# Optimization experiments

Hardware: AMD Instinct MI355X
Metric: run time of the kernel (lower is better)

## Reference

```python
import jax, jax.numpy as jnp
import numpy as np

EPS = 1e-12  # torch F.normalize default eps


def setup_inputs() -> dict:
    key = jax.random.key(0)
    ks = jax.random.split(key, 4)
    b, c, h, w = 2, 192, 256, 256
    num_heads = 4
    x = jax.random.normal(ks[0], (b, c, h, w), dtype=jnp.float32)
    w_qkv = jax.random.normal(ks[1], (3 * c, c), dtype=jnp.float32) * 0.02
    w_dw = jax.random.normal(ks[2], (3 * c, 1, 3, 3), dtype=jnp.float32) * 0.1
    w_proj = jax.random.normal(ks[3], (c, c), dtype=jnp.float32) * 0.02
    temperature = jnp.ones((num_heads, 1, 1), dtype=jnp.float32)
    return {"x": x, "w_qkv": w_qkv, "w_dw": w_dw, "w_proj": w_proj,
            "temperature": temperature, "num_heads": num_heads}


def reference(x, w_qkv, w_dw, w_proj, temperature, num_heads):
    b, c, h, w = x.shape
    ch = c // num_heads
    # 1x1 conv (pointwise GEMM) then depthwise 3x3 conv
    qkv = jnp.einsum('bchw,oc->bohw', x, w_qkv)
    qkv = jax.lax.conv_general_dilated(
        qkv, w_dw, window_strides=(1, 1), padding='SAME',
        dimension_numbers=('NCHW', 'OIHW', 'NCHW'),
        feature_group_count=3 * c)
    q, k, v = jnp.split(qkv, 3, axis=1)
    # b (head c) h w -> b head (c h) w
    def to_heads(t):
        return t.reshape(b, num_heads, ch * h, w)
    q, k, v = to_heads(q), to_heads(k), to_heads(v)
    # L2-normalize over the (c h) axis
    def l2n(t):
        n = jnp.sqrt(jnp.sum(t * t, axis=-2, keepdims=True))
        return t / jnp.maximum(n, EPS)
    q, k = l2n(q), l2n(k)
    # channel-transposed attention over width: attn is (b, head, w, w)
    attn = jnp.einsum('bhcw,bhcv->bhwv', q, k) * temperature[None]
    attn = jax.nn.softmax(attn, axis=-2)  # softmax over dim=-2 as in source
    out = jnp.einsum('bhcw,bhwv->bhcv', v, attn)
    out = out.reshape(b, c, h, w)
    return jnp.einsum('bchw,oc->bohw', out, w_proj)
```

## Files before the change

kernel.cpp:

```cpp
#include <hip/hip_runtime.h>
#include <math.h>

#define HW 65536

typedef float f32x4 __attribute__((ext_vector_type(4)));
typedef short bf16x8 __attribute__((ext_vector_type(8)));
typedef short bf16x4 __attribute__((ext_vector_type(4)));

static constexpr size_t OFF_A0    = 0;
static constexpr size_t OFF_SP    = 50331648;
static constexpr size_t OFF_VOUTT = 100663296;
static constexpr size_t OFF_XQK   = 150994944;
static constexpr size_t OFF_VPL   = 251658240;
static constexpr size_t OFF_PT    = 301989888;
static constexpr size_t OFF_NORMS = 303038464;
static constexpr size_t OFF_WQ    = 303054848;
static constexpr size_t OFF_WP    = 303276032;

__device__ inline float b2f(unsigned short u) { union { unsigned u; float f; } v; v.u = ((unsigned)u) << 16; return v.f; }
__device__ inline unsigned short f2b(float f) {
    union { float f; unsigned u; } v; v.f = f;
    return (unsigned short)((v.u + 0x7fffu + ((v.u >> 16) & 1u)) >> 16);
}

__global__ __launch_bounds__(256) void conv_w(const float* __restrict__ wq, const float* __restrict__ wp,
                                              unsigned short* __restrict__ wqb, unsigned short* __restrict__ wpb)
{
    int t = blockIdx.x * 256 + threadIdx.x;
    int stride = gridDim.x * 256;
    for (int i = t; i < 576 * 192; i += stride) wqb[i] = f2b(wq[i]);
    for (int i = t; i < 192 * 192; i += stride) wpb[i] = f2b(wp[i]);
}

__global__ __launch_bounds__(256) void conv_x(const float* __restrict__ x, unsigned short* __restrict__ xb)
{
    __shared__ unsigned short T[64 * 200];
    int tid = threadIdx.x;
    int b = blockIdx.y;
    long p0 = (long)blockIdx.x * 64;
#pragma unroll
    for (int it = 0; it < 12; ++it) {
        int c = it * 16 + (tid >> 4);
        int px = (tid & 15) * 4;
        float4 v = *(const float4*)(x + ((long)b * 192 + c) * HW + p0 + px);
        T[(px + 0) * 200 + c] = f2b(v.x);
        T[(px + 1) * 200 + c] = f2b(v.y);
        T[(px + 2) * 200 + c] = f2b(v.z);
        T[(px + 3) * 200 + c] = f2b(v.w);
    }
    __syncthreads();
    int px = tid >> 2, q = tid & 3;
    unsigned short* ob = xb + ((long)b * HW + p0 + px) * 192 + q * 48;
#pragma unroll
    for (int e = 0; e < 6; ++e)
        *(bf16x8*)(ob + e * 8) = *(const bf16x8*)&T[px * 200 + q * 48 + e * 8];
}

__global__ __launch_bounds__(256) void gemm_pm2(const unsigned short* __restrict__ Aw,
                                                const unsigned short* __restrict__ Bp,
                                                unsigned short* __restrict__ outb,
                                                float* __restrict__ outf, int Mtiles)
{
    __shared__ unsigned short Bs[128 * 200];
    int tid = threadIdx.x;
    int w = tid >> 6, lane = tid & 63, lg = lane >> 4, li = lane & 15;
    int wm = w >> 1, wn = w & 1;
    long pflat = (long)blockIdx.x * 128;

#pragma unroll
    for (int it = 0; it < 12; ++it) {
        int f = it * 256 + tid;
        int row = f / 24, cs = (f % 24) * 8;
        *(bf16x8*)&Bs[row * 200 + cs] = *(const bf16x8*)(Bp + (pflat + row) * 192 + cs);
    }
    __syncthreads();

    bf16x8 Bf[4][6];
#pragma unroll
    for (int fb = 0; fb < 4; ++fb)
#pragma unroll
        for (int ks = 0; ks < 6; ++ks)
            Bf[fb][ks] = *(const bf16x8*)&Bs[(wn * 64 + fb * 16 + li) * 200 + ks * 32 + lg * 8];

    const int b = (int)(blockIdx.x >> 9);
    const int pxl = ((int)blockIdx.x & 511) * 128 + wn * 64;
    const int Mtot = Mtiles * 64;

    for (int mt = 0; mt < Mtiles; ++mt) {
        int oc0 = mt * 64;
        const unsigned short* ab = Aw + (long)(oc0 + wm * 32 + li) * 192 + lg * 8;
        f32x4 acc[2][4];
#pragma unroll
        for (int i = 0; i < 2; ++i)
#pragma unroll
            for (int j = 0; j < 4; ++j) acc[i][j] = (f32x4){0.f, 0.f, 0.f, 0.f};
#pragma unroll
        for (int ks = 0; ks < 6; ++ks) {
            bf16x8 a0 = *(const bf16x8*)(ab + ks * 32);
            bf16x8 a1 = *(const bf16x8*)(ab + 16 * 192 + ks * 32);
#pragma unroll
            for (int fb = 0; fb < 4; ++fb) {
                acc[0][fb] = __builtin_amdgcn_mfma_f32_16x16x32_bf16(a0, Bf[fb][ks], acc[0][fb], 0, 0, 0);
                acc[1][fb] = __builtin_amdgcn_mfma_f32_16x16x32_bf16(a1, Bf[fb][ks], acc[1][fb], 0, 0, 0);
            }
        }
#pragma unroll
        for (int fa = 0; fa < 2; ++fa) {
            int m = oc0 + wm * 32 + fa * 16 + lg * 4;
#pragma unroll
            for (int fb = 0; fb < 4; ++fb) {
                int px = pxl + fb * 16 + li;
                long base = ((long)b * Mtot + m) * HW + px;
#pragma unroll
                for (int ii = 0; ii < 4; ++ii) {
                    if (outf) outf[base + (long)ii * HW] = acc[fa][fb][ii];
                    else      outb[base + (long)ii * HW] = f2b(acc[fa][fb][ii]);
                }
            }
        }
    }
}

__global__ __launch_bounds__(256) void dwconv2(const unsigned short* __restrict__ in,
                                               const float* __restrict__ wdw,
                                               unsigned short* __restrict__ qkT,
                                               unsigned short* __restrict__ vpl)
{
    __shared__ unsigned short Ls[34 * 272];
    int tid = threadIdx.x;
    int zp = blockIdx.y;
    int b = zp / 576, ch3 = zp % 576;
    int y0 = blockIdx.x * 32;
    const unsigned short* ip = in + (long)zp * HW;
    float w9[9];
#pragma unroll
    for (int t = 0; t < 9; ++t) w9[t] = wdw[ch3 * 9 + t];

    const bf16x8 z8 = (bf16x8){0, 0, 0, 0, 0, 0, 0, 0};
    if (tid < 34)               *(bf16x8*)&Ls[tid * 272] = z8;
    else if (tid < 68)          *(bf16x8*)&Ls[(tid - 34) * 272 + 264] = z8;
#pragma unroll
    for (int it = 0; it < 5; ++it) {
        int task = it * 256 + tid;
        if (task < 1088) {
            int r = task >> 5, seg = task & 31;
            int gy = y0 - 1 + r;
            bf16x8 v = z8;
            if (gy >= 0 && gy < 256) v = *(const bf16x8*)(ip + gy * 256 + seg * 8);
            *(bf16x8*)&Ls[r * 272 + 8 + seg * 8] = v;
        }
    }
    __syncthreads();

    int xg = tid & 63, yg = tid >> 6;
    int x0 = xg * 4;
    float acc[8][4];
#pragma unroll
    for (int yy = 0; yy < 8; ++yy)
#pragma unroll
        for (int xi = 0; xi < 4; ++xi) acc[yy][xi] = 0.f;

#pragma unroll
    for (int rr = 0; rr < 10; ++rr) {
        const unsigned short* lp = &Ls[(yg * 8 + rr) * 272 + 8 + x0];
        bf16x4 A  = *(const bf16x4*)(lp - 4);
        bf16x4 Bv = *(const bf16x4*)(lp);
        bf16x4 Cv = *(const bf16x4*)(lp + 4);
        float f[6] = { b2f((unsigned short)A[3]),  b2f((unsigned short)Bv[0]),
                       b2f((unsigned short)Bv[1]), b2f((unsigned short)Bv[2]),
                       b2f((unsigned short)Bv[3]), b2f((unsigned short)Cv[0]) };
#pragma unroll
        for (int dy = 0; dy < 3; ++dy) {
            int yy = rr - dy;
            if (yy >= 0 && yy < 8) {
#pragma unroll
                for (int dx = 0; dx < 3; ++dx)
#pragma unroll
                    for (int xi = 0; xi < 4; ++xi)
                        acc[yy][xi] = fmaf(w9[dy * 3 + dx], f[dx + xi], acc[yy][xi]);
            }
        }
    }

    if (ch3 < 384) {
        int isk = ch3 >= 192 ? 1 : 0;
        int chq = ch3 - isk * 192;
        int hh = chq / 48, cc = chq % 48;
        long zbase = (long)(b * 8 + isk * 4 + hh) * 3145728L + (long)cc * 256 + y0 + yg * 8;
#pragma unroll
        for (int xi = 0; xi < 4; ++xi) {
            bf16x8 pv;
#pragma unroll
            for (int yy = 0; yy < 8; ++yy) pv[yy] = (short)f2b(acc[yy][xi]);
            *(bf16x8*)(qkT + zbase + (long)(x0 + xi) * 12288) = pv;
        }
    } else {
        unsigned short* ob = vpl + (long)(b * 192 + ch3 - 384) * HW + (long)(y0 + yg * 8) * 256 + x0;
#pragma unroll
        for (int yy = 0; yy < 8; ++yy) {
            bf16x4 pv;
#pragma unroll
            for (int xi = 0; xi < 4; ++xi) pv[xi] = (short)f2b(acc[yy][xi]);
            *(bf16x4*)(ob + yy * 256) = pv;
        }
    }
}

__global__ __launch_bounds__(256) void transpose_bf16(const unsigned short* __restrict__ src,
                                                      unsigned short* __restrict__ dst, int mode)
{
    __shared__ unsigned short T[64][72];
    int tid = threadIdx.x;
    int z = blockIdx.z;
    long so, dofs; int R, C;
    if (mode == 0) {
        int b = z >> 3, isk = (z >> 2) & 1, h = z & 3;
        so = ((long)(b * 576 + isk * 192 + h * 48)) * HW;
        dofs = (long)z * 12288 * 256;
        R = 12288; C = 256;
    } else {
        so = (long)z * 192 * HW;
        dofs = (long)z * HW * 192;
        R = 192; C = HW;
    }
    int r0 = blockIdx.y * 64, c0 = blockIdx.x * 64;
#pragma unroll
    for (int rr = 0; rr < 2; ++rr) {
        int r = rr * 32 + (tid >> 3);
        int cs = (tid & 7) * 8;
        *(bf16x8*)&T[r][cs] = *(const bf16x8*)(src + so + (long)(r0 + r) * C + c0 + cs);
    }
    __syncthreads();
#pragma unroll
    for (int cc = 0; cc < 2; ++cc) {
        int c = cc * 32 + (tid >> 3);
        int rs = (tid & 7) * 8;
        bf16x8 v;
#pragma unroll
        for (int e = 0; e < 8; ++e) v[e] = (short)T[rs + e][c];
        *(bf16x8*)(dst + dofs + (long)(c0 + c) * R + r0 + rs) = v;
    }
}

__global__ __launch_bounds__(256) void norms_k(const unsigned short* __restrict__ qkT, float* __restrict__ norms)
{
    int i = blockIdx.x, z = blockIdx.y;
    const unsigned short* p = qkT + ((long)z * 256 + i) * 12288 + threadIdx.x * 8;
    float s = 0.f;
#pragma unroll
    for (int it = 0; it < 6; ++it) {
        bf16x8 v = *(const bf16x8*)(p + it * 2048);
#pragma unroll
        for (int e = 0; e < 8; ++e) { float f = b2f((unsigned short)v[e]); s = fmaf(f, f, s); }
    }
    for (int off = 32; off > 0; off >>= 1) s += __shfl_down(s, off, 64);
    __shared__ float r4[4];
    if ((threadIdx.x & 63) == 0) r4[threadIdx.x >> 6] = s;
    __syncthreads();
    if (threadIdx.x == 0) {
        float t = r4[0] + r4[1] + r4[2] + r4[3];
        norms[z * 256 + i] = 1.0f / fmaxf(sqrtf(t), 1e-12f);
    }
}

__global__ __launch_bounds__(256) void attn_qk(const unsigned short* __restrict__ qkT, float* __restrict__ Sp)
{
    __shared__ unsigned short Qs[128 * 40];
    __shared__ unsigned short Ks[128 * 40];
    int tid = threadIdx.x;
    int z = blockIdx.z; int bh = z >> 4, sk = z & 15; int b = bh >> 2, h = bh & 3;
    const unsigned short* qT = qkT + (long)(b * 8 + h) * 3145728;
    const unsigned short* kT = qkT + (long)(b * 8 + 4 + h) * 3145728;
    int i0 = blockIdx.x * 128, j0 = blockIdx.y * 128;
    int w = tid >> 6, lane = tid & 63, lg = lane >> 4, li = lane & 15;
    int wm = w >> 1, wn = w & 1;
    int srow = tid >> 2, sseg = (tid & 3) * 8;
    long qoff = (long)(i0 + srow) * 12288 + sk * 768 + sseg;
    long koff = (long)(j0 + srow) * 12288 + sk * 768 + sseg;

    f32x4 acc[4][4];
#pragma unroll
    for (int i = 0; i < 4; ++i)
#pragma unroll
        for (int j = 0; j < 4; ++j) acc[i][j] = (f32x4){0.f, 0.f, 0.f, 0.f};

    bf16x8 qr0 = *(const bf16x8*)(qT + qoff);
    bf16x8 qr1 = *(const bf16x8*)(qT + qoff + (long)64 * 12288);
    bf16x8 kr0 = *(const bf16x8*)(kT + koff);
    bf16x8 kr1 = *(const bf16x8*)(kT + koff + (long)64 * 12288);

#pragma unroll 1
    for (int ks = 0; ks < 24; ++ks) {
        *(bf16x8*)&Qs[srow * 40 + sseg] = qr0;
        *(bf16x8*)&Qs[(64 + srow) * 40 + sseg] = qr1;
        *(bf16x8*)&Ks[srow * 40 + sseg] = kr0;
        *(bf16x8*)&Ks[(64 + srow) * 40 + sseg] = kr1;
        if (ks < 23) {
            long o = (long)(ks + 1) * 32;
            qr0 = *(const bf16x8*)(qT + qoff + o);
            qr1 = *(const bf16x8*)(qT + qoff + (long)64 * 12288 + o);
            kr0 = *(const bf16x8*)(kT + koff + o);
            kr1 = *(const bf16x8*)(kT + koff + (long)64 * 12288 + o);
        }
        __syncthreads();
        bf16x8 af[4], bfr[4];
#pragma unroll
        for (int fa = 0; fa < 4; ++fa)
            af[fa] = *(const bf16x8*)&Qs[(wm * 64 + fa * 16 + li) * 40 + lg * 8];
#pragma unroll
        for (int fb = 0; fb < 4; ++fb)
            bfr[fb] = *(const bf16x8*)&Ks[(wn * 64 + fb * 16 + li) * 40 + lg * 8];
#pragma unroll
        for (int fa = 0; fa < 4; ++fa)
#pragma unroll
            for (int fb = 0; fb < 4; ++fb)
                acc[fa][fb] = __builtin_amdgcn_mfma_f32_16x16x32_bf16(af[fa], bfr[fb], acc[fa][fb], 0, 0, 0);
        __syncthreads();
    }

    float* op = Sp + ((long)(sk * 8 + bh) << 16);
#pragma unroll
    for (int fa = 0; fa < 4; ++fa) {
        int i = i0 + wm * 64 + fa * 16 + lg * 4;
#pragma unroll
        for (int fb = 0; fb < 4; ++fb) {
            int j = j0 + wn * 64 + fb * 16 + li;
#pragma unroll
            for (int ii = 0; ii < 4; ++ii)
                op[(long)(i + ii) * 256 + j] = acc[fa][fb][ii];
        }
    }
}

__global__ __launch_bounds__(256) void softmax_k(const float* __restrict__ Sp, const float* __restrict__ norms,
                                                 const float* __restrict__ temp, unsigned short* __restrict__ Pt)
{
    __shared__ float Sd[256 * 9];
    __shared__ float red[32 * 9];
    int tid = threadIdx.x;
    int g = blockIdx.x; int bh = g >> 5, jq = g & 31; int b = bh >> 2, h = bh & 3;
    int jl = tid & 7, iq = tid >> 3;
    int j = jq * 8 + jl;
    const float* nq = norms + (b * 8 + h) * 256;
    float invkj = norms[(b * 8 + 4 + h) * 256 + j] * temp[h];
    const float* sp = Sp + (long)bh * HW + j;

    float m = -1e30f;
#pragma unroll
    for (int ii = 0; ii < 8; ++ii) {
        int i = iq * 8 + ii;
        float s = 0.f;
#pragma unroll
        for (int sk = 0; sk < 16; ++sk) s += sp[((long)(sk * 8) << 16) + i * 256];
        float v = s * nq[i] * invkj;
        Sd[i * 9 + jl] = v;
        m = fmaxf(m, v);
    }
    red[iq * 9 + jl] = m;
    __syncthreads();
    m = -1e30f;
#pragma unroll
    for (int s2 = 0; s2 < 32; ++s2) m = fmaxf(m, red[s2 * 9 + jl]);
    __syncthreads();
    float sum = 0.f;
#pragma unroll
    for (int ii = 0; ii < 8; ++ii) sum += __expf(Sd[(iq * 8 + ii) * 9 + jl] - m);
    red[iq * 9 + jl] = sum;
    __syncthreads();
    sum = 0.f;
#pragma unroll
    for (int s2 = 0; s2 < 32; ++s2) sum += red[s2 * 9 + jl];
    float rs = 1.0f / sum;

    int fb = jq >> 1, li2 = (jq & 1) * 8 + jl;
    int ks = iq >> 2, lg = iq & 3;
    unsigned short* pt = Pt + (long)bh * HW + (long)((fb * 8 + ks) * 64 + lg * 16 + li2) * 8;
    bf16x8 pv;
#pragma unroll
    for (int ii = 0; ii < 8; ++ii)
        pv[ii] = (short)f2b(__expf(Sd[(iq * 8 + ii) * 9 + jl] - m) * rs);
    *(bf16x8*)pt = pv;
}

__global__ __launch_bounds__(256) void vattn(const unsigned short* __restrict__ vpl,
                                             const unsigned short* __restrict__ Pt,
                                             unsigned short* __restrict__ vout)
{
    int tid = threadIdx.x;
    int w = tid >> 6, lane = tid & 63, lg = lane >> 4, li = lane & 15;
    int wm = w >> 1, wn = w & 1;
    int m0 = blockIdx.x * 64 + wm * 32;
    int bh = blockIdx.y; int b = bh >> 2, h = bh & 3;
    const unsigned short* V = vpl + (long)(b * 192 + h * 48) * HW;
    const unsigned short* P = Pt + (long)bh * HW + wn * 32768 + lane * 8;

    f32x4 acc[2][8];
#pragma unroll
    for (int i = 0; i < 2; ++i)
#pragma unroll
        for (int j = 0; j < 8; ++j) acc[i][j] = (f32x4){0.f, 0.f, 0.f, 0.f};

#pragma unroll 2
    for (int ks = 0; ks < 8; ++ks) {
        bf16x8 a0 = *(const bf16x8*)(V + (long)(m0 + li) * 256 + ks * 32 + lg * 8);
        bf16x8 a1 = *(const bf16x8*)(V + (long)(m0 + 16 + li) * 256 + ks * 32 + lg * 8);
#pragma unroll
        for (int fb2 = 0; fb2 < 8; ++fb2) {
            bf16x8 bb = *(const bf16x8*)(P + (fb2 * 8 + ks) * 512);
            acc[0][fb2] = __builtin_amdgcn_mfma_f32_16x16x32_bf16(a0, bb, acc[0][fb2], 0, 0, 0);
            acc[1][fb2] = __builtin_amdgcn_mfma_f32_16x16x32_bf16(a1, bb, acc[1][fb2], 0, 0, 0);
        }
    }
    unsigned short* ob = vout + (long)(b * 192 + h * 48) * HW;
#pragma unroll
    for (int fa = 0; fa < 2; ++fa) {
#pragma unroll
        for (int fb2 = 0; fb2 < 8; ++fb2) {
            int j = (wn * 8 + fb2) * 16 + li;
#pragma unroll
            for (int ii = 0; ii < 4; ++ii) {
                int m = m0 + fa * 16 + lg * 4 + ii;
                ob[((long)(m >> 8) << 16) + ((m & 255) << 8) + j] = f2b(acc[fa][fb2][ii]);
            }
        }
    }
}

extern "C" void kernel_launch(void* const* d_in, const int* in_sizes, int n_in,
                              void* d_out, int out_size, void* d_ws, size_t ws_size,
                              hipStream_t stream)
{
    (void)in_sizes; (void)n_in; (void)out_size; (void)ws_size;
    const float* x      = (const float*)d_in[0];
    const float* w_qkv  = (const float*)d_in[1];
    const float* w_dw   = (const float*)d_in[2];
    const float* w_proj = (const float*)d_in[3];
    const float* temp   = (const float*)d_in[4];
    float* out = (float*)d_out;
    char* ws = (char*)d_ws;

    unsigned short* qkv_pre = (unsigned short*)(ws + OFF_A0);
    unsigned short* vout    = (unsigned short*)(ws + OFF_A0);
    float*          Sp      = (float*)(ws + OFF_SP);
    unsigned short* voutT   = (unsigned short*)(ws + OFF_VOUTT);
    unsigned short* xb      = (unsigned short*)(ws + OFF_XQK);
    unsigned short* qkT     = (unsigned short*)(ws + OFF_XQK);
    unsigned short* vpl     = (unsigned short*)(ws + OFF_VPL);
    unsigned short* Pt      = (unsigned short*)(ws + OFF_PT);
    float*          norms   = (float*)(ws + OFF_NORMS);
    unsigned short* wqb     = (unsigned short*)(ws + OFF_WQ);
    unsigned short* wpb     = (unsigned short*)(ws + OFF_WP);

    conv_w<<<64, 256, 0, stream>>>(w_qkv, w_proj, wqb, wpb);
    conv_x<<<dim3(1024, 2), 256, 0, stream>>>(x, xb);
    gemm_pm2<<<1024, 256, 0, stream>>>(wqb, xb, qkv_pre, nullptr, 9);
    dwconv2<<<dim3(8, 1152), 256, 0, stream>>>(qkv_pre, w_dw, qkT, vpl);
    norms_k<<<dim3(256, 16), 256, 0, stream>>>(qkT, norms);
    attn_qk<<<dim3(2, 2, 128), 256, 0, stream>>>(qkT, Sp);
    softmax_k<<<256, 256, 0, stream>>>(Sp, norms, temp, Pt);
    vattn<<<dim3(192, 8), 256, 0, stream>>>(vpl, Pt, vout);
    transpose_bf16<<<dim3(1024, 3, 2), 256, 0, stream>>>(vout, voutT, 1);
    gemm_pm2<<<1024, 256, 0, stream>>>(wpb, voutT, nullptr, out, 3);
}
```

Before: 349.8 us.

## Fuse q/k norm reduction into dwconv epilogue and widen attn_qk tiles

The depthwise conv kernel now computes per-column squared sums of the q/k outputs from its fp32 accumulators, reduces them in shared memory and atomically adds them into a zeroed buffer. A tiny finalize kernel then turns these into inverse norms, replacing the separate norms kernel that re-read all of qkT. attn_qk is also reshaped to 512-thread blocks covering all 256 key columns, so each Q tile is loaded once instead of twice. The cost is extra barriers and atomics in dwconv, plus a larger shared-memory footprint and fewer blocks in attn_qk. Norms now come from unrounded fp32 values, a slight numerical change.

```diff
diff --git a/kernel.cpp b/kernel.cpp
--- a/kernel.cpp
+++ b/kernel.cpp
@@ -7,15 +7,16 @@
 typedef short bf16x8 __attribute__((ext_vector_type(8)));
 typedef short bf16x4 __attribute__((ext_vector_type(4)));
 
-static constexpr size_t OFF_A0    = 0;
-static constexpr size_t OFF_SP    = 50331648;
-static constexpr size_t OFF_VOUTT = 100663296;
-static constexpr size_t OFF_XQK   = 150994944;
-static constexpr size_t OFF_VPL   = 251658240;
-static constexpr size_t OFF_PT    = 301989888;
-static constexpr size_t OFF_NORMS = 303038464;
-static constexpr size_t OFF_WQ    = 303054848;
-static constexpr size_t OFF_WP    = 303276032;
+static constexpr size_t OFF_A0     = 0;
+static constexpr size_t OFF_SP     = 50331648;
+static constexpr size_t OFF_VOUTT  = 100663296;
+static constexpr size_t OFF_XQK    = 150994944;
+static constexpr size_t OFF_VPL    = 251658240;
+static constexpr size_t OFF_PT     = 301989888;
+static constexpr size_t OFF_NORMP  = 303038464;
+static constexpr size_t OFF_WQ     = 303054848;
+static constexpr size_t OFF_WP     = 303276032;
+static constexpr size_t OFF_NORMS  = 303349760;
 
 __device__ inline float b2f(unsigned short u) { union { unsigned u; float f; } v; v.u = ((unsigned)u) << 16; return v.f; }
 __device__ inline unsigned short f2b(float f) {
@@ -124,7 +125,8 @@
 __global__ __launch_bounds__(256) void dwconv2(const unsigned short* __restrict__ in,
                                                const float* __restrict__ wdw,
                                                unsigned short* __restrict__ qkT,
-                                               unsigned short* __restrict__ vpl)
+                                               unsigned short* __restrict__ vpl,
+                                               float* __restrict__ normp)
 {
     __shared__ unsigned short Ls[34 * 272];
     int tid = threadIdx.x;
@@ -186,7 +188,8 @@
         int isk = ch3 >= 192 ? 1 : 0;
         int chq = ch3 - isk * 192;
         int hh = chq / 48, cc = chq % 48;
-        long zbase = (long)(b * 8 + isk * 4 + hh) * 3145728L + (long)cc * 256 + y0 + yg * 8;
+        int z2 = b * 8 + isk * 4 + hh;
+        long zbase = (long)z2 * 3145728L + (long)cc * 256 + y0 + yg * 8;
 #pragma unroll
         for (int xi = 0; xi < 4; ++xi) {
             bf16x8 pv;
@@ -194,6 +197,27 @@
             for (int yy = 0; yy < 8; ++yy) pv[yy] = (short)f2b(acc[yy][xi]);
             *(bf16x8*)(qkT + zbase + (long)(x0 + xi) * 12288) = pv;
         }
+        float s[4];
+#pragma unroll
+        for (int xi = 0; xi < 4; ++xi) {
+            float t = 0.f;
+#pragma unroll
+            for (int yy = 0; yy < 8; ++yy) t = fmaf(acc[yy][xi], acc[yy][xi], t);
+            s[xi] = t;
+        }
+        __syncthreads();
+        float* colsq = (float*)Ls;
+#pragma unroll
+        for (int xi = 0; xi < 4; ++xi) colsq[yg * 256 + x0 + xi] = s[xi];
+        __syncthreads();
+        if (yg == 0) {
+#pragma unroll
+            for (int xi = 0; xi < 4; ++xi) {
+                float t = colsq[x0 + xi] + colsq[256 + x0 + xi] +
+                          colsq[512 + x0 + xi] + colsq[768 + x0 + xi];
+                atomicAdd(&normp[z2 * 256 + x0 + xi], t);
+            }
+        }
     } else {
         unsigned short* ob = vpl + (long)(b * 192 + ch3 - 384) * HW + (long)(y0 + yg * 8) * 256 + x0;
 #pragma unroll
@@ -204,6 +228,12 @@
             *(bf16x4*)(ob + yy * 256) = pv;
         }
     }
+}
+
+__global__ __launch_bounds__(256) void norms_fin(const float* __restrict__ normp, float* __restrict__ norms)
+{
+    int x = threadIdx.x, g = blockIdx.x;
+    norms[g * 256 + x] = 1.0f / fmaxf(sqrtf(normp[g * 256 + x]), 1e-12f);
 }
 
 __global__ __launch_bounds__(256) void transpose_bf16(const unsigned short* __restrict__ src,
@@ -242,41 +272,22 @@
     }
 }
 
-__global__ __launch_bounds__(256) void norms_k(const unsigned short* __restrict__ qkT, float* __restrict__ norms)
-{
-    int i = blockIdx.x, z = blockIdx.y;
-    const unsigned short* p = qkT + ((long)z * 256 + i) * 12288 + threadIdx.x * 8;
-    float s = 0.f;
-#pragma unroll
-    for (int it = 0; it < 6; ++it) {
-        bf16x8 v = *(const bf16x8*)(p + it * 2048);
-#pragma unroll
-        for (int e = 0; e < 8; ++e) { float f = b2f((unsigned short)v[e]); s = fmaf(f, f, s); }
-    }
-    for (int off = 32; off > 0; off >>= 1) s += __shfl_down(s, off, 64);
-    __shared__ float r4[4];
-    if ((threadIdx.x & 63) == 0) r4[threadIdx.x >> 6] = s;
-    __syncthreads();
-    if (threadIdx.x == 0) {
-        float t = r4[0] + r4[1] + r4[2] + r4[3];
-        norms[z * 256 + i] = 1.0f / fmaxf(sqrtf(t), 1e-12f);
-    }
-}
-
-__global__ __launch_bounds__(256) void attn_qk(const unsigned short* __restrict__ qkT, float* __restrict__ Sp)
+__global__ __launch_bounds__(512, 4) void attn_qk(const unsigned short* __restrict__ qkT, float* __restrict__ Sp)
 {
     __shared__ unsigned short Qs[128 * 40];
-    __shared__ unsigned short Ks[128 * 40];
+    __shared__ unsigned short Ks[256 * 40];
     int tid = threadIdx.x;
     int z = blockIdx.z; int bh = z >> 4, sk = z & 15; int b = bh >> 2, h = bh & 3;
     const unsigned short* qT = qkT + (long)(b * 8 + h) * 3145728;
     const unsigned short* kT = qkT + (long)(b * 8 + 4 + h) * 3145728;
-    int i0 = blockIdx.x * 128, j0 = blockIdx.y * 128;
+    int i0 = blockIdx.x * 128;
     int w = tid >> 6, lane = tid & 63, lg = lane >> 4, li = lane & 15;
-    int wm = w >> 1, wn = w & 1;
-    int srow = tid >> 2, sseg = (tid & 3) * 8;
-    long qoff = (long)(i0 + srow) * 12288 + sk * 768 + sseg;
-    long koff = (long)(j0 + srow) * 12288 + sk * 768 + sseg;
+    int wm = w >> 2, wn = w & 3;
+    int rq = tid >> 2, seg = (tid & 3) * 8;
+
+    const unsigned short* qp  = qT + (long)(i0 + rq) * 12288 + sk * 768 + seg;
+    const unsigned short* kp1 = kT + (long)rq * 12288 + sk * 768 + seg;
+    const unsigned short* kp2 = kT + (long)(128 + rq) * 12288 + sk * 768 + seg;
 
     f32x4 acc[4][4];
 #pragma unroll
@@ -284,23 +295,20 @@
 #pragma unroll
         for (int j = 0; j < 4; ++j) acc[i][j] = (f32x4){0.f, 0.f, 0.f, 0.f};
 
-    bf16x8 qr0 = *(const bf16x8*)(qT + qoff);
-    bf16x8 qr1 = *(const bf16x8*)(qT + qoff + (long)64 * 12288);
-    bf16x8 kr0 = *(const bf16x8*)(kT + koff);
-    bf16x8 kr1 = *(const bf16x8*)(kT + koff + (long)64 * 12288);
+    bf16x8 qr = *(const bf16x8*)qp;
+    bf16x8 kr1 = *(const bf16x8*)kp1;
+    bf16x8 kr2 = *(const bf16x8*)kp2;
 
 #pragma unroll 1
     for (int ks = 0; ks < 24; ++ks) {
-        *(bf16x8*)&Qs[srow * 40 + sseg] = qr0;
-        *(bf16x8*)&Qs[(64 + srow) * 40 + sseg] = qr1;
-        *(bf16x8*)&Ks[srow * 40 + sseg] = kr0;
-        *(bf16x8*)&Ks[(64 + srow) * 40 + sseg] = kr1;
+        *(bf16x8*)&Qs[rq * 40 + seg] = qr;
+        *(bf16x8*)&Ks[rq * 40 + seg] = kr1;
+        *(bf16x8*)&Ks[(128 + rq) * 40 + seg] = kr2;
         if (ks < 23) {
             long o = (long)(ks + 1) * 32;
-            qr0 = *(const bf16x8*)(qT + qoff + o);
-            qr1 = *(const bf16x8*)(qT + qoff + (long)64 * 12288 + o);
-            kr0 = *(const bf16x8*)(kT + koff + o);
-            kr1 = *(const bf16x8*)(kT + koff + (long)64 * 12288 + o);
+            qr  = *(const bf16x8*)(qp + o);
+            kr1 = *(const bf16x8*)(kp1 + o);
+            kr2 = *(const bf16x8*)(kp2 + o);
         }
         __syncthreads();
         bf16x8 af[4], bfr[4];
@@ -324,7 +332,7 @@
         int i = i0 + wm * 64 + fa * 16 + lg * 4;
 #pragma unroll
         for (int fb = 0; fb < 4; ++fb) {
-            int j = j0 + wn * 64 + fb * 16 + li;
+            int j = wn * 64 + fb * 16 + li;
 #pragma unroll
             for (int ii = 0; ii < 4; ++ii)
                 op[(long)(i + ii) * 256 + j] = acc[fa][fb][ii];
@@ -447,16 +455,18 @@
     unsigned short* qkT     = (unsigned short*)(ws + OFF_XQK);
     unsigned short* vpl     = (unsigned short*)(ws + OFF_VPL);
     unsigned short* Pt      = (unsigned short*)(ws + OFF_PT);
+    float*          normp   = (float*)(ws + OFF_NORMP);
     float*          norms   = (float*)(ws + OFF_NORMS);
     unsigned short* wqb     = (unsigned short*)(ws + OFF_WQ);
     unsigned short* wpb     = (unsigned short*)(ws + OFF_WP);
 
     conv_w<<<64, 256, 0, stream>>>(w_qkv, w_proj, wqb, wpb);
     conv_x<<<dim3(1024, 2), 256, 0, stream>>>(x, xb);
+    hipMemsetAsync(normp, 0, 16384, stream);
     gemm_pm2<<<1024, 256, 0, stream>>>(wqb, xb, qkv_pre, nullptr, 9);
-    dwconv2<<<dim3(8, 1152), 256, 0, stream>>>(qkv_pre, w_dw, qkT, vpl);
-    norms_k<<<dim3(256, 16), 256, 0, stream>>>(qkT, norms);
-    attn_qk<<<dim3(2, 2, 128), 256, 0, stream>>>(qkT, Sp);
+    dwconv2<<<dim3(8, 1152), 256, 0, stream>>>(qkv_pre, w_dw, qkT, vpl, normp);
+    norms_fin<<<16, 256, 0, stream>>>(normp, norms);
+    attn_qk<<<dim3(2, 1, 128), 512, 0, stream>>>(qkT, Sp);
     softmax_k<<<256, 256, 0, stream>>>(Sp, norms, temp, Pt);
     vattn<<<dim3(192, 8), 256, 0, stream>>>(vpl, Pt, vout);
     transpose_bf16<<<dim3(1024, 3, 2), 256, 0, stream>>>(vout, voutT, 1);
```

Measured after the change: 407.0 us. 1.16x slower.
